# Performance work log

Measured on AMD Instinct MI355X. Metric: run time of the kernel, lower is better.

## Reference

```python
import jax, jax.numpy as jnp
import numpy as np
import math

NEG = -9e15
NOISE_SCALE = 0.4

def _gat(h, A, a0, a1, a2, a3):
    # e_k[b,i,j] = leakyrelu(sum_d h[b,i,d]*h[b,j,d]*a_k[d])  (== (h[i]*h[j]) @ a_k)
    def score(a):
        return jax.nn.leaky_relu(jnp.einsum('bid,bjd->bij', h * a, h), 0.2)
    e0, e1, e2, e3 = score(a0), score(a1), score(a2), score(a3)
    alpha = jnp.where(A == 1, e0, NEG)
    alpha = jnp.where(A == 2, e1, alpha)
    alpha = jnp.where(A == 3, e2, alpha)
    alpha = jnp.where(A == 4, e3, alpha)
    alpha = jax.nn.softmax(alpha, axis=-1)
    return jnp.einsum('bij,bjd->bid', alpha, h)

def _ave_pooling(h, mask):
    length = jnp.sum(mask, axis=1)                      # [B]
    return jnp.sum(h * mask[:, :, None], axis=1) / length[:, None]

def _att_pooling(h, star, mask):
    sim = jnp.exp(jnp.einsum('bnd,bd->bn', h, star))    # [B,N]
    sim = sim * mask
    sim = sim / (jnp.sum(sim, axis=-1, keepdims=True) + 1e-24)
    return jnp.sum(sim[:, :, None] * h, axis=1)         # [B,D]

def _forward(A, hidden, graph_mask, a0, a1, a2, a3, noise):
    step, D = noise.shape[0], hidden.shape[-1]
    star = _ave_pooling(hidden, graph_mask)
    embs = []
    for i in range(step):
        hidden = _gat(hidden, A, a0, a1, a2, a3)
        sim = jnp.einsum('bnd,bd->bn', hidden, star) / math.sqrt(D)
        alpha = jax.nn.sigmoid(sim)[:, :, None]
        hidden = (1.0 - alpha) * hidden + alpha * star[:, None, :]
        n = noise[i]
        n = n / jnp.maximum(jnp.linalg.norm(n, axis=-1, keepdims=True), 1e-12)
        hidden = hidden + jnp.sign(hidden) * n * NOISE_SCALE
        star = _att_pooling(hidden, star, graph_mask)
        embs.append(hidden)
    embeddings_cl = jnp.mean(jnp.stack(embs, axis=1), axis=1)
    return hidden, star, embeddings_cl

def setup_inputs() -> dict:
    key = jax.random.key(0)
    ks = jax.random.split(key, 8)
    B, N, D, STEP = 256, 128, 512, 3
    A = jax.random.randint(ks[0], (B, N, N), 0, 5, dtype=jnp.int64)
    hidden = jax.random.normal(ks[1], (B, N, D), dtype=jnp.float32)
    graph_mask = jnp.ones((B, N), dtype=jnp.float32)
    a0 = jax.random.normal(ks[2], (D,), dtype=jnp.float32) * 0.1
    a1 = jax.random.normal(ks[3], (D,), dtype=jnp.float32) * 0.1
    a2 = jax.random.normal(ks[4], (D,), dtype=jnp.float32) * 0.1
    a3 = jax.random.normal(ks[5], (D,), dtype=jnp.float32) * 0.1
    noise = jax.random.uniform(ks[6], (STEP, B, N, D), dtype=jnp.float32)
    return {"A": A, "hidden": hidden, "graph_mask": graph_mask,
            "a0": a0, "a1": a1, "a2": a2, "a3": a3, "noise": noise}

def reference(A, hidden, graph_mask, a0, a1, a2, a3, noise):
    return _forward(A, hidden, graph_mask, a0, a1, a2, a3, noise)
```

## Files before the change

### kernel.cpp

```cpp
#include <hip/hip_runtime.h>
#include <math.h>

#define BB 256
#define NN 128
#define DD 512
#define NEGV (-9e15f)

__global__ __launch_bounds__(256) void k_avepool(const float* __restrict__ h,
                                                 const float* __restrict__ mask,
                                                 float* __restrict__ star) {
    const int b = blockIdx.x;
    const int t = threadIdx.x;
    const float* hb = h + (size_t)b * NN * DD;
    const float* mb = mask + (size_t)b * NN;
    float acc0 = 0.f, acc1 = 0.f, L = 0.f;
    for (int n = 0; n < NN; ++n) {
        float m = mb[n];
        L += m;
        acc0 += m * hb[n * DD + t];
        acc1 += m * hb[n * DD + t + 256];
    }
    star[b * DD + t] = acc0 / L;
    star[b * DD + t + 256] = acc1 / L;
}

__global__ __launch_bounds__(1024, 1) void k_gat(const float* __restrict__ h_in,
                                                 const int* __restrict__ A,
                                                 const float* __restrict__ a0,
                                                 const float* __restrict__ a1,
                                                 const float* __restrict__ a2,
                                                 const float* __restrict__ a3,
                                                 float* __restrict__ h_gat) {
    __shared__ float4 hA[NN * 17];
    __shared__ float4 hB[NN * 17];
    __shared__ float  eselS[NN * 132];

    const int tid = threadIdx.x;
    const int b = blockIdx.x;
    const float* __restrict__ hb = h_in + (size_t)b * NN * DD;

    const bool hasJob = tid < 544;
    int jjb = 0, jr = 0;
    if (hasJob) {
        int rem = tid;
        for (int k = 0; k < 16; ++k) {
            int c = 4 * k + 4;
            if (rem < c) { jjb = k; jr = rem; break; }
            rem -= c;
        }
    }
    const int i0 = jr * 2, i1 = i0 + 1;
    const int jb8 = jjb * 8;
    const int swi = (jr >> 2) & 7;
    const int swj = jjb & 7;

    auto stageAll = [&](float4* buf, int d0) {
        #pragma unroll
        for (int q = 0; q < 2; ++q) {
            int l = q * 1024 + tid;
            int row = l >> 4, c4 = l & 15;
            buf[row * 17 + (c4 ^ ((row >> 3) & 7))] = *(const float4*)(hb + row * DD + d0 + c4 * 4);
        }
    };

    float acc0[8][4], acc1[8][4];
    #pragma unroll
    for (int jj = 0; jj < 8; ++jj)
        #pragma unroll
        for (int k = 0; k < 4; ++k) { acc0[jj][k] = 0.f; acc1[jj][k] = 0.f; }

    stageAll(hA, 0);
    __syncthreads();
    for (int ck = 0; ck < 8; ++ck) {
        const int d0 = ck * 64;
        const float4* cur = (ck & 1) ? hB : hA;
        float4* nxt = (ck & 1) ? hA : hB;
        if (ck < 7) stageAll(nxt, d0 + 64);
        if (hasJob) {
            #pragma unroll 2
            for (int c4 = 0; c4 < 16; ++c4) {
                const int dbase = d0 + c4 * 4;
                const float av0x = a0[dbase],     av0y = a1[dbase],     av0z = a2[dbase],     av0w = a3[dbase];
                const float av1x = a0[dbase + 1], av1y = a1[dbase + 1], av1z = a2[dbase + 1], av1w = a3[dbase + 1];
                const float av2x = a0[dbase + 2], av2y = a1[dbase + 2], av2z = a2[dbase + 2], av2w = a3[dbase + 2];
                const float av3x = a0[dbase + 3], av3y = a1[dbase + 3], av3z = a2[dbase + 3], av3w = a3[dbase + 3];
                float4 hi0 = cur[i0 * 17 + (c4 ^ swi)];
                float4 hi1 = cur[i1 * 17 + (c4 ^ swi)];
                #pragma unroll
                for (int jj = 0; jj < 8; ++jj) {
                    float4 hj = cur[(jb8 + jj) * 17 + (c4 ^ swj)];
                    float p;
                    p = hi0.x * hj.x; acc0[jj][0] += p * av0x; acc0[jj][1] += p * av0y; acc0[jj][2] += p * av0z; acc0[jj][3] += p * av0w;
                    p = hi0.y * hj.y; acc0[jj][0] += p * av1x; acc0[jj][1] += p * av1y; acc0[jj][2] += p * av1z; acc0[jj][3] += p * av1w;
                    p = hi0.z * hj.z; acc0[jj][0] += p * av2x; acc0[jj][1] += p * av2y; acc0[jj][2] += p * av2z; acc0[jj][3] += p * av2w;
                    p = hi0.w * hj.w; acc0[jj][0] += p * av3x; acc0[jj][1] += p * av3y; acc0[jj][2] += p * av3z; acc0[jj][3] += p * av3w;
                    p = hi1.x * hj.x; acc1[jj][0] += p * av0x; acc1[jj][1] += p * av0y; acc1[jj][2] += p * av0z; acc1[jj][3] += p * av0w;
                    p = hi1.y * hj.y; acc1[jj][0] += p * av1x; acc1[jj][1] += p * av1y; acc1[jj][2] += p * av1z; acc1[jj][3] += p * av1w;
                    p = hi1.z * hj.z; acc1[jj][0] += p * av2x; acc1[jj][1] += p * av2y; acc1[jj][2] += p * av2z; acc1[jj][3] += p * av2w;
                    p = hi1.w * hj.w; acc1[jj][0] += p * av3x; acc1[jj][1] += p * av3y; acc1[jj][2] += p * av3z; acc1[jj][3] += p * av3w;
                }
            }
        }
        __syncthreads();
    }

    {
        auto selv = [](const float* a4, int Av) -> float {
            float e = (Av == 1) ? a4[0] : (Av == 2) ? a4[1] : (Av == 3) ? a4[2] : a4[3];
            float lr = (e > 0.f) ? e : 0.2f * e;
            return (Av >= 1 && Av <= 4) ? lr : NEGV;
        };
        if (hasJob) {
            const int* __restrict__ Ab = A + (size_t)b * NN * NN;
            #pragma unroll
            for (int jj = 0; jj < 8; ++jj) {
                const int j = jb8 + jj;
                int Av;
                Av = Ab[i0 * NN + j];  eselS[i0 * 132 + j] = selv(acc0[jj], Av);
                Av = Ab[i1 * NN + j];  eselS[i1 * 132 + j] = selv(acc1[jj], Av);
                Av = Ab[j * NN + i0];  eselS[j * 132 + i0] = selv(acc0[jj], Av);
                Av = Ab[j * NN + i1];  eselS[j * 132 + i1] = selv(acc1[jj], Av);
            }
        }
        __syncthreads();
    }

    {
        const int it4 = tid >> 8;
        const int sub = tid & 255;
        const int ti = sub >> 4, tj = sub & 15;
        const int li0 = it4 * 32 + ti * 2, li1 = li0 + 1;
        float s0[8], s1[8];
        #pragma unroll
        for (int jj = 0; jj < 8; ++jj) {
            s0[jj] = eselS[li0 * 132 + tj + 16 * jj];
            s1[jj] = eselS[li1 * 132 + tj + 16 * jj];
        }
        float m0 = s0[0], m1 = s1[0];
        #pragma unroll
        for (int jj = 1; jj < 8; ++jj) { m0 = fmaxf(m0, s0[jj]); m1 = fmaxf(m1, s1[jj]); }
        #pragma unroll
        for (int off = 1; off < 16; off <<= 1) {
            m0 = fmaxf(m0, __shfl_xor(m0, off));
            m1 = fmaxf(m1, __shfl_xor(m1, off));
        }
        float e0[8], e1[8], sum0 = 0.f, sum1 = 0.f;
        #pragma unroll
        for (int jj = 0; jj < 8; ++jj) {
            e0[jj] = expf(s0[jj] - m0); sum0 += e0[jj];
            e1[jj] = expf(s1[jj] - m1); sum1 += e1[jj];
        }
        #pragma unroll
        for (int off = 1; off < 16; off <<= 1) {
            sum0 += __shfl_xor(sum0, off);
            sum1 += __shfl_xor(sum1, off);
        }
        #pragma unroll
        for (int jj = 0; jj < 8; ++jj) {
            eselS[li0 * 132 + tj + 16 * jj] = e0[jj] / sum0;
            eselS[li1 * 132 + tj + 16 * jj] = e1[jj] / sum1;
        }
    }
    __syncthreads();

    stageAll(hA, 0);
    __syncthreads();
    const int gd = tid & 15, jh = (tid >> 4) & 1, rg = tid >> 5;
    const int r0p = rg * 8;
    const int jbase = jh * 64;
#define PVROW(r, ac) { s[r].x += (ac) * hv.x; s[r].y += (ac) * hv.y; s[r].z += (ac) * hv.z; s[r].w += (ac) * hv.w; }
    for (int ck = 0; ck < 8; ++ck) {
        const int d0 = ck * 64;
        const float4* cur = (ck & 1) ? hB : hA;
        float4* nxt = (ck & 1) ? hA : hB;
        if (tid >= 512) {
            if (ck < 7) {
                #pragma unroll
                for (int q = 0; q < 4; ++q) {
                    int l = q * 512 + (tid - 512);
                    int row = l >> 4, c4 = l & 15;
                    nxt[row * 17 + (c4 ^ ((row >> 3) & 7))] = *(const float4*)(hb + row * DD + d0 + 64 + c4 * 4);
                }
            }
        } else {
            float4 s[8];
            #pragma unroll
            for (int r = 0; r < 8; ++r) s[r] = make_float4(0.f, 0.f, 0.f, 0.f);
            #pragma unroll 2
            for (int jq = 0; jq < 16; ++jq) {
                const int j0 = jbase + jq * 4;
                const int swz = (j0 >> 3) & 7;
                float4 av0 = *(const float4*)(&eselS[(r0p + 0) * 132 + j0]);
                float4 av1 = *(const float4*)(&eselS[(r0p + 1) * 132 + j0]);
                float4 av2 = *(const float4*)(&eselS[(r0p + 2) * 132 + j0]);
                float4 av3 = *(const float4*)(&eselS[(r0p + 3) * 132 + j0]);
                float4 av4 = *(const float4*)(&eselS[(r0p + 4) * 132 + j0]);
                float4 av5 = *(const float4*)(&eselS[(r0p + 5) * 132 + j0]);
                float4 av6 = *(const float4*)(&eselS[(r0p + 6) * 132 + j0]);
                float4 av7 = *(const float4*)(&eselS[(r0p + 7) * 132 + j0]);
                float4 hv;
                hv = cur[(j0 + 0) * 17 + (gd ^ swz)];
                PVROW(0, av0.x) PVROW(1, av1.x) PVROW(2, av2.x) PVROW(3, av3.x)
                PVROW(4, av4.x) PVROW(5, av5.x) PVROW(6, av6.x) PVROW(7, av7.x)
                hv = cur[(j0 + 1) * 17 + (gd ^ swz)];
                PVROW(0, av0.y) PVROW(1, av1.y) PVROW(2, av2.y) PVROW(3, av3.y)
                PVROW(4, av4.y) PVROW(5, av5.y) PVROW(6, av6.y) PVROW(7, av7.y)
                hv = cur[(j0 + 2) * 17 + (gd ^ swz)];
                PVROW(0, av0.z) PVROW(1, av1.z) PVROW(2, av2.z) PVROW(3, av3.z)
                PVROW(4, av4.z) PVROW(5, av5.z) PVROW(6, av6.z) PVROW(7, av7.z)
                hv = cur[(j0 + 3) * 17 + (gd ^ swz)];
                PVROW(0, av0.w) PVROW(1, av1.w) PVROW(2, av2.w) PVROW(3, av3.w)
                PVROW(4, av4.w) PVROW(5, av5.w) PVROW(6, av6.w) PVROW(7, av7.w)
            }
            #pragma unroll
            for (int r = 0; r < 8; ++r) {
                float mx = __shfl_xor(s[r].x, 16);
                float my = __shfl_xor(s[r].y, 16);
                float mz = __shfl_xor(s[r].z, 16);
                float mw = __shfl_xor(s[r].w, 16);
                s[r].x += mx; s[r].y += my; s[r].z += mz; s[r].w += mw;
            }
            if (jh == 0) {
                float* outp = h_gat + ((size_t)b * NN + r0p) * DD + d0 + gd * 4;
                #pragma unroll
                for (int r = 0; r < 8; ++r) *(float4*)(outp + (size_t)r * DD) = s[r];
            }
        }
        __syncthreads();
    }
#undef PVROW
}

__global__ __launch_bounds__(256) void k_mix(const float* __restrict__ h_gat,
                                             const float* __restrict__ star,
                                             const float* __restrict__ noise_s,
                                             float* __restrict__ h_out,
                                             float* __restrict__ embs,
                                             int first) {
    const int b = blockIdx.y;
    const int tid = threadIdx.x;
    const int wave = tid >> 6, lane = tid & 63;
    const int row0 = blockIdx.x * 16 + wave * 4;
    const float* stp = star + (size_t)b * DD + lane * 8;
    float4 st0 = *(const float4*)(stp);
    float4 st1 = *(const float4*)(stp + 4);
    const float inv3 = 1.0f / 3.0f;

    for (int rr = 0; rr < 4; ++rr) {
        const int row = row0 + rr;
        const size_t base = ((size_t)b * NN + row) * DD + lane * 8;
        float4 hg0 = *(const float4*)(h_gat + base);
        float4 hg1 = *(const float4*)(h_gat + base + 4);
        float4 n0 = *(const float4*)(noise_s + base);
        float4 n1 = *(const float4*)(noise_s + base + 4);
        float dot = hg0.x*st0.x + hg0.y*st0.y + hg0.z*st0.z + hg0.w*st0.w
                  + hg1.x*st1.x + hg1.y*st1.y + hg1.z*st1.z + hg1.w*st1.w;
        float nn = n0.x*n0.x + n0.y*n0.y + n0.z*n0.z + n0.w*n0.w
                 + n1.x*n1.x + n1.y*n1.y + n1.z*n1.z + n1.w*n1.w;
        #pragma unroll
        for (int off = 1; off < 64; off <<= 1) {
            dot += __shfl_xor(dot, off);
            nn  += __shfl_xor(nn, off);
        }
        const float sim = dot / 22.62741699796952f;
        const float al = 1.0f / (1.0f + expf(-sim));
        const float ns = 0.4f / fmaxf(sqrtf(nn), 1e-12f);

        float hm, sg, hn[8];
        float hgv[8] = {hg0.x,hg0.y,hg0.z,hg0.w,hg1.x,hg1.y,hg1.z,hg1.w};
        float stv[8] = {st0.x,st0.y,st0.z,st0.w,st1.x,st1.y,st1.z,st1.w};
        float nv [8] = {n0.x,n0.y,n0.z,n0.w,n1.x,n1.y,n1.z,n1.w};
        #pragma unroll
        for (int c = 0; c < 8; ++c) {
            hm = (1.0f - al) * hgv[c] + al * stv[c];
            sg = (hm > 0.f) ? 1.f : ((hm < 0.f) ? -1.f : 0.f);
            hn[c] = hm + sg * nv[c] * ns;
        }
        float4 w0 = make_float4(hn[0], hn[1], hn[2], hn[3]);
        float4 w1 = make_float4(hn[4], hn[5], hn[6], hn[7]);
        *(float4*)(h_out + base) = w0;
        *(float4*)(h_out + base + 4) = w1;
        if (first) {
            float4 ea = make_float4(hn[0]*inv3, hn[1]*inv3, hn[2]*inv3, hn[3]*inv3);
            float4 eb = make_float4(hn[4]*inv3, hn[5]*inv3, hn[6]*inv3, hn[7]*inv3);
            *(float4*)(embs + base) = ea;
            *(float4*)(embs + base + 4) = eb;
        } else {
            float4 ea = *(const float4*)(embs + base);
            float4 eb = *(const float4*)(embs + base + 4);
            ea.x += hn[0]*inv3; ea.y += hn[1]*inv3; ea.z += hn[2]*inv3; ea.w += hn[3]*inv3;
            eb.x += hn[4]*inv3; eb.y += hn[5]*inv3; eb.z += hn[6]*inv3; eb.w += hn[7]*inv3;
            *(float4*)(embs + base) = ea;
            *(float4*)(embs + base + 4) = eb;
        }
    }
}

__global__ __launch_bounds__(256) void k_attpool(const float* __restrict__ h,
                                                 const float* __restrict__ star_in,
                                                 const float* __restrict__ mask,
                                                 float* __restrict__ star_out) {
    __shared__ float starS[DD];
    __shared__ float simS[NN];
    __shared__ float wS[NN];
    __shared__ float sh_M, sh_inv;
    const int b = blockIdx.x;
    const int tid = threadIdx.x;
    starS[tid] = star_in[b * DD + tid];
    starS[tid + 256] = star_in[b * DD + tid + 256];
    __syncthreads();
    const int wave = tid >> 6, lane = tid & 63;
    const float* hb = h + (size_t)b * NN * DD;
    float4 sv0 = *(const float4*)(&starS[lane * 8]);
    float4 sv1 = *(const float4*)(&starS[lane * 8 + 4]);
    for (int q = 0; q < 32; ++q) {
        const int n = wave * 32 + q;
        const float* hr = hb + n * DD + lane * 8;
        float4 h0 = *(const float4*)(hr);
        float4 h1 = *(const float4*)(hr + 4);
        float dot = h0.x*sv0.x + h0.y*sv0.y + h0.z*sv0.z + h0.w*sv0.w
                  + h1.x*sv1.x + h1.y*sv1.y + h1.z*sv1.z + h1.w*sv1.w;
        #pragma unroll
        for (int off = 1; off < 64; off <<= 1) dot += __shfl_xor(dot, off);
        if (lane == 0) simS[n] = dot;
    }
    __syncthreads();
    if (tid < 64) {
        float v = fmaxf(simS[tid], simS[tid + 64]);
        #pragma unroll
        for (int off = 1; off < 64; off <<= 1) v = fmaxf(v, __shfl_xor(v, off));
        if (tid == 0) sh_M = v;
    }
    __syncthreads();
    const float M = sh_M;
    if (tid < NN) wS[tid] = expf(simS[tid] - M) * mask[b * NN + tid];
    __syncthreads();
    if (tid < 64) {
        float v = wS[tid] + wS[tid + 64];
        #pragma unroll
        for (int off = 1; off < 64; off <<= 1) v += __shfl_xor(v, off);
        if (tid == 0) sh_inv = 1.0f / (v + 1e-24f * expf(-M));
    }
    __syncthreads();
    const float inv = sh_inv;
    float acc0 = 0.f, acc1 = 0.f;
    for (int n = 0; n < NN; ++n) {
        const float w = wS[n];
        acc0 += w * hb[n * DD + tid];
        acc1 += w * hb[n * DD + tid + 256];
    }
    star_out[b * DD + tid] = acc0 * inv;
    star_out[b * DD + tid + 256] = acc1 * inv;
}

extern "C" void kernel_launch(void* const* d_in, const int* in_sizes, int n_in,
                              void* d_out, int out_size, void* d_ws, size_t ws_size,
                              hipStream_t stream) {
    const int*   A      = (const int*)d_in[0];
    const float* hidden = (const float*)d_in[1];
    const float* mask   = (const float*)d_in[2];
    const float* a0     = (const float*)d_in[3];
    const float* a1     = (const float*)d_in[4];
    const float* a2     = (const float*)d_in[5];
    const float* a3     = (const float*)d_in[6];
    const float* noise  = (const float*)d_in[7];

    float* out_h    = (float*)d_out;
    float* out_star = out_h + (size_t)BB * NN * DD;
    float* out_embs = out_star + (size_t)BB * DD;

    float* ws_h    = (float*)d_ws;
    float* ws_star = ws_h + (size_t)BB * NN * DD;

    k_avepool<<<BB, 256, 0, stream>>>(hidden, mask, ws_star);

    for (int s = 0; s < 3; ++s) {
        const float* hin = (s == 0) ? hidden : ws_h;
        k_gat<<<BB, 1024, 0, stream>>>(hin, A, a0, a1, a2, a3, out_h);
        const float* ns = noise + (size_t)s * BB * NN * DD;
        float* hout = (s == 2) ? out_h : ws_h;
        k_mix<<<dim3(8, BB), 256, 0, stream>>>(out_h, ws_star, ns, hout, out_embs, (s == 0) ? 1 : 0);
        float* so = (s == 2) ? out_star : ws_star;
        k_attpool<<<BB, 256, 0, stream>>>(hout, ws_star, mask, so);
    }
}
```

Before: 969.9 us.

## Fuse mix and attention pooling into one kernel and defer embedding averaging

Merges the mix/noise kernel and the attention-pooling kernel into a single per-batch 1024-thread kernel. It computes the pooling similarity from registers and then re-reads the freshly written hidden rows, which are likely still in cache, for the weighted sum. When the workspace is large enough, the per-step hidden states are kept in two buffers and the embedding mean is written once in the last step, replacing the per-step read-modify-write of the embeddings. The GAT PV stage also remaps each thread's rows to an interleaved stride-2 pattern, probably to change LDS access conflicts. The cost is extra workspace and lower parallelism in the post kernel, with one block per batch instead of eight.

After: 1.489 ms. 1.54x slower.

```diff
diff --git a/kernel.cpp b/kernel.cpp
--- a/kernel.cpp
+++ b/kernel.cpp
@@ -165,8 +165,8 @@
 
     stageAll(hA, 0);
     __syncthreads();
-    const int gd = tid & 15, jh = (tid >> 4) & 1, rg = tid >> 5;
-    const int r0p = rg * 8;
+    const int gd = tid & 15, jh = (tid >> 4) & 1, rsub = (tid >> 5) & 1, wv = tid >> 6;
+    const int rbase = wv * 16 + rsub;
     const int jbase = jh * 64;
 #define PVROW(r, ac) { s[r].x += (ac) * hv.x; s[r].y += (ac) * hv.y; s[r].z += (ac) * hv.z; s[r].w += (ac) * hv.w; }
     for (int ck = 0; ck < 8; ++ck) {
@@ -190,14 +190,14 @@
             for (int jq = 0; jq < 16; ++jq) {
                 const int j0 = jbase + jq * 4;
                 const int swz = (j0 >> 3) & 7;
-                float4 av0 = *(const float4*)(&eselS[(r0p + 0) * 132 + j0]);
-                float4 av1 = *(const float4*)(&eselS[(r0p + 1) * 132 + j0]);
-                float4 av2 = *(const float4*)(&eselS[(r0p + 2) * 132 + j0]);
-                float4 av3 = *(const float4*)(&eselS[(r0p + 3) * 132 + j0]);
-                float4 av4 = *(const float4*)(&eselS[(r0p + 4) * 132 + j0]);
-                float4 av5 = *(const float4*)(&eselS[(r0p + 5) * 132 + j0]);
-                float4 av6 = *(const float4*)(&eselS[(r0p + 6) * 132 + j0]);
-                float4 av7 = *(const float4*)(&eselS[(r0p + 7) * 132 + j0]);
+                float4 av0 = *(const float4*)(&eselS[(rbase +  0) * 132 + j0]);
+                float4 av1 = *(const float4*)(&eselS[(rbase +  2) * 132 + j0]);
+                float4 av2 = *(const float4*)(&eselS[(rbase +  4) * 132 + j0]);
+                float4 av3 = *(const float4*)(&eselS[(rbase +  6) * 132 + j0]);
+                float4 av4 = *(const float4*)(&eselS[(rbase +  8) * 132 + j0]);
+                float4 av5 = *(const float4*)(&eselS[(rbase + 10) * 132 + j0]);
+                float4 av6 = *(const float4*)(&eselS[(rbase + 12) * 132 + j0]);
+                float4 av7 = *(const float4*)(&eselS[(rbase + 14) * 132 + j0]);
                 float4 hv;
                 hv = cur[(j0 + 0) * 17 + (gd ^ swz)];
                 PVROW(0, av0.x) PVROW(1, av1.x) PVROW(2, av2.x) PVROW(3, av3.x)
@@ -221,9 +221,9 @@
                 s[r].x += mx; s[r].y += my; s[r].z += mz; s[r].w += mw;
             }
             if (jh == 0) {
-                float* outp = h_gat + ((size_t)b * NN + r0p) * DD + d0 + gd * 4;
+                float* outp = h_gat + ((size_t)b * NN + rbase) * DD + d0 + gd * 4;
                 #pragma unroll
-                for (int r = 0; r < 8; ++r) *(float4*)(outp + (size_t)r * DD) = s[r];
+                for (int r = 0; r < 8; ++r) *(float4*)(outp + (size_t)(2 * r) * DD) = s[r];
             }
         }
         __syncthreads();
@@ -231,23 +231,30 @@
 #undef PVROW
 }
 
-__global__ __launch_bounds__(256) void k_mix(const float* __restrict__ h_gat,
-                                             const float* __restrict__ star,
-                                             const float* __restrict__ noise_s,
-                                             float* __restrict__ h_out,
-                                             float* __restrict__ embs,
-                                             int first) {
-    const int b = blockIdx.y;
+__global__ __launch_bounds__(1024) void k_post(const float* __restrict__ h_gat,
+                                               const float* __restrict__ star,
+                                               const float* __restrict__ noise_s,
+                                               const float* __restrict__ mask,
+                                               const float* __restrict__ h1p,
+                                               const float* __restrict__ h2p,
+                                               float* __restrict__ h_out,
+                                               float* __restrict__ star_out,
+                                               float* __restrict__ embs,
+                                               int mode) {
+    __shared__ float simS[NN];
+    __shared__ float wS[NN];
+    __shared__ float sh_M, sh_inv;
+
     const int tid = threadIdx.x;
+    const int b = blockIdx.x;
     const int wave = tid >> 6, lane = tid & 63;
-    const int row0 = blockIdx.x * 16 + wave * 4;
     const float* stp = star + (size_t)b * DD + lane * 8;
     float4 st0 = *(const float4*)(stp);
     float4 st1 = *(const float4*)(stp + 4);
     const float inv3 = 1.0f / 3.0f;
 
-    for (int rr = 0; rr < 4; ++rr) {
-        const int row = row0 + rr;
+    for (int p = 0; p < 8; ++p) {
+        const int row = wave * 8 + p;
         const size_t base = ((size_t)b * NN + row) * DD + lane * 8;
         float4 hg0 = *(const float4*)(h_gat + base);
         float4 hg1 = *(const float4*)(h_gat + base + 4);
@@ -276,55 +283,48 @@
             sg = (hm > 0.f) ? 1.f : ((hm < 0.f) ? -1.f : 0.f);
             hn[c] = hm + sg * nv[c] * ns;
         }
-        float4 w0 = make_float4(hn[0], hn[1], hn[2], hn[3]);
-        float4 w1 = make_float4(hn[4], hn[5], hn[6], hn[7]);
-        *(float4*)(h_out + base) = w0;
-        *(float4*)(h_out + base + 4) = w1;
-        if (first) {
-            float4 ea = make_float4(hn[0]*inv3, hn[1]*inv3, hn[2]*inv3, hn[3]*inv3);
-            float4 eb = make_float4(hn[4]*inv3, hn[5]*inv3, hn[6]*inv3, hn[7]*inv3);
-            *(float4*)(embs + base) = ea;
-            *(float4*)(embs + base + 4) = eb;
-        } else {
+        *(float4*)(h_out + base)     = make_float4(hn[0], hn[1], hn[2], hn[3]);
+        *(float4*)(h_out + base + 4) = make_float4(hn[4], hn[5], hn[6], hn[7]);
+
+        float d2 = hn[0]*stv[0] + hn[1]*stv[1] + hn[2]*stv[2] + hn[3]*stv[3]
+                 + hn[4]*stv[4] + hn[5]*stv[5] + hn[6]*stv[6] + hn[7]*stv[7];
+        #pragma unroll
+        for (int off = 1; off < 64; off <<= 1) d2 += __shfl_xor(d2, off);
+        if (lane == 0) simS[row] = d2;
+
+        if (mode == 1) {
+            float4 a0v = *(const float4*)(h1p + base);
+            float4 a1v = *(const float4*)(h1p + base + 4);
+            float4 b0v = *(const float4*)(h2p + base);
+            float4 b1v = *(const float4*)(h2p + base + 4);
+            float h1v[8] = {a0v.x,a0v.y,a0v.z,a0v.w,a1v.x,a1v.y,a1v.z,a1v.w};
+            float h2v[8] = {b0v.x,b0v.y,b0v.z,b0v.w,b1v.x,b1v.y,b1v.z,b1v.w};
+            float ev[8];
+            #pragma unroll
+            for (int c = 0; c < 8; ++c) {
+                float e = h1v[c] * inv3;
+                e += h2v[c] * inv3;
+                e += hn[c] * inv3;
+                ev[c] = e;
+            }
+            *(float4*)(embs + base)     = make_float4(ev[0], ev[1], ev[2], ev[3]);
+            *(float4*)(embs + base + 4) = make_float4(ev[4], ev[5], ev[6], ev[7]);
+        } else if (mode == 2) {
+            *(float4*)(embs + base)     = make_float4(hn[0]*inv3, hn[1]*inv3, hn[2]*inv3, hn[3]*inv3);
+            *(float4*)(embs + base + 4) = make_float4(hn[4]*inv3, hn[5]*inv3, hn[6]*inv3, hn[7]*inv3);
+        } else if (mode == 3) {
             float4 ea = *(const float4*)(embs + base);
             float4 eb = *(const float4*)(embs + base + 4);
             ea.x += hn[0]*inv3; ea.y += hn[1]*inv3; ea.z += hn[2]*inv3; ea.w += hn[3]*inv3;
             eb.x += hn[4]*inv3; eb.y += hn[5]*inv3; eb.z += hn[6]*inv3; eb.w += hn[7]*inv3;
-            *(float4*)(embs + base) = ea;
+            *(float4*)(embs + base)     = ea;
             *(float4*)(embs + base + 4) = eb;
         }
     }
-}
-
-__global__ __launch_bounds__(256) void k_attpool(const float* __restrict__ h,
-                                                 const float* __restrict__ star_in,
-                                                 const float* __restrict__ mask,
-                                                 float* __restrict__ star_out) {
-    __shared__ float starS[DD];
-    __shared__ float simS[NN];
-    __shared__ float wS[NN];
-    __shared__ float sh_M, sh_inv;
-    const int b = blockIdx.x;
-    const int tid = threadIdx.x;
-    starS[tid] = star_in[b * DD + tid];
-    starS[tid + 256] = star_in[b * DD + tid + 256];
-    __syncthreads();
-    const int wave = tid >> 6, lane = tid & 63;
-    const float* hb = h + (size_t)b * NN * DD;
-    float4 sv0 = *(const float4*)(&starS[lane * 8]);
-    float4 sv1 = *(const float4*)(&starS[lane * 8 + 4]);
-    for (int q = 0; q < 32; ++q) {
-        const int n = wave * 32 + q;
-        const float* hr = hb + n * DD + lane * 8;
-        float4 h0 = *(const float4*)(hr);
-        float4 h1 = *(const float4*)(hr + 4);
-        float dot = h0.x*sv0.x + h0.y*sv0.y + h0.z*sv0.z + h0.w*sv0.w
-                  + h1.x*sv1.x + h1.y*sv1.y + h1.z*sv1.z + h1.w*sv1.w;
-        #pragma unroll
-        for (int off = 1; off < 64; off <<= 1) dot += __shfl_xor(dot, off);
-        if (lane == 0) simS[n] = dot;
-    }
-    __syncthreads();
+
+    __threadfence();
+    __syncthreads();
+
     if (tid < 64) {
         float v = fmaxf(simS[tid], simS[tid + 64]);
         #pragma unroll
@@ -343,14 +343,13 @@
     }
     __syncthreads();
     const float inv = sh_inv;
-    float acc0 = 0.f, acc1 = 0.f;
-    for (int n = 0; n < NN; ++n) {
-        const float w = wS[n];
-        acc0 += w * hb[n * DD + tid];
-        acc1 += w * hb[n * DD + tid + 256];
-    }
-    star_out[b * DD + tid] = acc0 * inv;
-    star_out[b * DD + tid + 256] = acc1 * inv;
+    if (tid < DD) {
+        const float* hb2 = h_out + (size_t)b * NN * DD;
+        float acc = 0.f;
+        for (int n = 0; n < NN; ++n)
+            acc += wS[n] * hb2[n * DD + tid];
+        star_out[b * DD + tid] = acc * inv;
+    }
 }
 
 extern "C" void kernel_launch(void* const* d_in, const int* in_sizes, int n_in,
@@ -369,18 +368,32 @@
     float* out_star = out_h + (size_t)BB * NN * DD;
     float* out_embs = out_star + (size_t)BB * DD;
 
-    float* ws_h    = (float*)d_ws;
-    float* ws_star = ws_h + (size_t)BB * NN * DD;
+    const size_t hElems = (size_t)BB * NN * DD;
+    const size_t needDeferred = (2 * hElems + (size_t)BB * DD) * sizeof(float);
+    const bool deferred = ws_size >= needDeferred;
+
+    float* ws_h1   = (float*)d_ws;
+    float* ws_h2   = deferred ? (ws_h1 + hElems) : ws_h1;
+    float* ws_star = deferred ? (ws_h2 + hElems) : (ws_h1 + hElems);
 
     k_avepool<<<BB, 256, 0, stream>>>(hidden, mask, ws_star);
 
     for (int s = 0; s < 3; ++s) {
-        const float* hin = (s == 0) ? hidden : ws_h;
+        const float* hin = (s == 0) ? hidden : (deferred ? ((s == 1) ? ws_h1 : ws_h2) : ws_h1);
         k_gat<<<BB, 1024, 0, stream>>>(hin, A, a0, a1, a2, a3, out_h);
+
         const float* ns = noise + (size_t)s * BB * NN * DD;
-        float* hout = (s == 2) ? out_h : ws_h;
-        k_mix<<<dim3(8, BB), 256, 0, stream>>>(out_h, ws_star, ns, hout, out_embs, (s == 0) ? 1 : 0);
-        float* so = (s == 2) ? out_star : ws_star;
-        k_attpool<<<BB, 256, 0, stream>>>(hout, ws_star, mask, so);
+        float* hout = (s == 2) ? out_h : (deferred ? ((s == 0) ? ws_h1 : ws_h2) : ws_h1);
+        float* sout = (s == 2) ? out_star : ws_star;
+        int mode;
+        const float* h1p = nullptr; const float* h2p = nullptr;
+        if (deferred) {
+            if (s < 2) mode = 0;
+            else { mode = 1; h1p = ws_h1; h2p = ws_h2; }
+        } else {
+            mode = (s == 0) ? 2 : 3;
+        }
+        k_post<<<BB, 1024, 0, stream>>>(out_h, ws_star, ns, mask, h1p, h2p,
+                                        hout, sout, out_embs, mode);
     }
 }
```
